# Performance work log

Measured on AMD Instinct MI355X. Metric: run time of the kernel, lower is better.

## Reference

```python
import jax, jax.numpy as jnp
import numpy as np

N_NODES = 50000

def cheb_conv(x, edge_index, W, b):
    # PyG ChebConv, K=2, normalization='sym', lambda_max=2.0 (default):
    # scaled Laplacian L_hat = (2/lambda_max)*L - I = -D^{-1/2} A D^{-1/2} (zero diag).
    # Tx_0 = x, Tx_1 = L_hat @ x ; out = Tx_0 @ W[0] + Tx_1 @ W[1] + b
    src, dst = edge_index[0], edge_index[1]
    ones = jnp.ones(src.shape[0], x.dtype)
    deg = jax.ops.segment_sum(ones, src, num_segments=N_NODES)
    dinv = jnp.where(deg > 0, 1.0 / jnp.sqrt(deg), 0.0)
    norm = -dinv[src] * dinv[dst]                                   # [E]
    tx1 = jax.ops.segment_sum(x[src] * norm[:, None], dst, num_segments=N_NODES)
    return x @ W[0] + tx1 @ W[1] + b

def setup_inputs() -> dict:
    key = jax.random.key(0)
    ks = jax.random.split(key, 12)
    IN, OUT, E, P = 128, 2, 800000, 400000
    return {
        "x": jax.random.normal(ks[0], (N_NODES, IN), jnp.float32),
        "edge_index": jax.random.randint(ks[1], (2, E), 0, N_NODES),
        "E_pos": jax.random.randint(ks[2], (2, P), 0, N_NODES),
        "neg_edge_index": jax.random.randint(ks[3], (2, P), 0, N_NODES),
        "W1": jax.random.normal(ks[4], (2, IN, 300), jnp.float32) * 0.05,
        "b1": jnp.zeros((300,), jnp.float32),
        "W2": jax.random.normal(ks[5], (2, 300, 100), jnp.float32) * 0.05,
        "b2": jnp.zeros((100,), jnp.float32),
        "W3": jax.random.normal(ks[6], (2, 100, OUT), jnp.float32) * 0.05,
        "b3": jnp.zeros((OUT,), jnp.float32),
        "lin1_W": jax.random.normal(ks[7], (100, IN), jnp.float32) * 0.05,
        "lin1_b": jnp.zeros((100,), jnp.float32),
        "lin2_W": jax.random.normal(ks[8], (100, IN), jnp.float32) * 0.05,
        "lin2_b": jnp.zeros((100,), jnp.float32),
        "c1": jnp.full((1,), 0.5, jnp.float32),
        "c2": jnp.full((1,), 0.5, jnp.float32),
    }

def reference(x, edge_index, E_pos, neg_edge_index, W1, b1, W2, b2, W3, b3,
              lin1_W, lin1_b, lin2_W, lin2_b, c1, c2):
    # eval mode: F.dropout and dropout_edge are identity
    x0 = x
    h = jax.nn.relu(cheb_conv(x0, edge_index, W1, b1))
    x1 = jax.nn.relu(cheb_conv(h, edge_index, W2, b2))
    x2 = x1 + jax.nn.relu(x0 @ lin1_W.T + lin1_b)
    z = x1 + jax.nn.relu(x0 @ lin2_W.T + lin2_b)
    pos_score = jnp.sum(z[E_pos[0]] * z[E_pos[1]], axis=1)              # [P]
    pos_loss = -jnp.mean(jnp.log(jax.nn.sigmoid(pos_score) + 1e-15))
    neg_score = jnp.sum(z[neg_edge_index[0]] * z[neg_edge_index[1]], axis=1)
    neg_loss = -jnp.mean(jnp.log(1.0 - jax.nn.sigmoid(neg_score) + 1e-15))
    r_loss = pos_loss + neg_loss
    out = cheb_conv(x2, edge_index, W3, b3)                             # [N, out_channels]
    return (out, r_loss, c1, c2)
```

## Files before the change

kernel.cpp:

```cpp
#include <hip/hip_runtime.h>
#include <math.h>


typedef unsigned short ushort_t;
typedef unsigned char u8;
typedef __attribute__((ext_vector_type(8))) __bf16 bf16x8;
typedef __attribute__((ext_vector_type(8))) short s16x8;
typedef __attribute__((ext_vector_type(4))) float f32x4;
typedef __attribute__((ext_vector_type(2))) float f32x2;

#define NB_H 64
#define HW 12500
#define PW 25000
#define LOSS_NB 1792

__device__ __forceinline__ f32x4 mfma16x16x32(s16x8 a, s16x8 b, f32x4 c) {
  return __builtin_amdgcn_mfma_f32_16x16x32_bf16(
      __builtin_bit_cast(bf16x8, a), __builtin_bit_cast(bf16x8, b), c, 0, 0, 0);
}
__device__ __forceinline__ ushort_t f2bf(float f) {
  union { float f; unsigned u; } c; c.f = f;
  unsigned r = (c.u + 0x7FFFu + ((c.u >> 16) & 1u)) >> 16;
  return (ushort_t)r;
}
__device__ __forceinline__ f32x2 cvt2lo(unsigned u) {
  return __builtin_amdgcn_cvt_pk_f32_fp8((int)u, false);
}
__device__ __forceinline__ f32x2 cvt2hi(unsigned u) {
  return __builtin_amdgcn_cvt_pk_f32_fp8((int)u, true);
}
__device__ __forceinline__ u8 f2fp8(float f) {
  return (u8)(__builtin_amdgcn_cvt_pk_fp8_f32(f, 0.f, 0, false) & 0xff);
}

template<int VAR, int NT, int KTOT>
__global__ __launch_bounds__(256) void gemm_mfma(
    const ushort_t* __restrict__ A0, const ushort_t* __restrict__ A1,
    const ushort_t* __restrict__ Wt,
    const float* __restrict__ bias0, const float* __restrict__ bias1,
    const float* __restrict__ x1,
    const float* __restrict__ W3c, const float* __restrict__ b3c,
    void* __restrict__ out0, void* __restrict__ out1,
    float* __restrict__ t0g, float* __restrict__ t1g, int M)
{
  constexpr int NF = NT / 32;
  __shared__ __align__(16) ushort_t As[64 * 40];
  __shared__ __align__(16) ushort_t Bs[NT * 40];
  __shared__ float w3s[400];
  const int tid  = threadIdx.x;
  const int lane = tid & 63, w = tid >> 6;
  const int m0 = blockIdx.x * 64;
  const int wm = (w & 1) * 32, wn = (w >> 1) * (NT / 2);
  if (VAR == 2) { for (int i = tid; i < 400; i += 256) w3s[i] = W3c[i]; }
  f32x4 acc[2][NF];
#pragma unroll
  for (int i = 0; i < 2; ++i)
#pragma unroll
    for (int j = 0; j < NF; ++j) acc[i][j] = (f32x4){0.f, 0.f, 0.f, 0.f};

  for (int k0 = 0; k0 < KTOT; k0 += 32) {
    {
      const int r = tid >> 2, c8 = (tid & 3) * 8;
      const int gm = m0 + r;
      uint4 v = {0u, 0u, 0u, 0u};
      if (gm < M) {
        if (VAR == 1) {
          const u8* s8 = (const u8*)A0 + (size_t)gm * 320 + k0 + c8;
          const uint2 r8 = *(const uint2*)s8;
          const f32x2 f0 = cvt2lo(r8.x), f1 = cvt2hi(r8.x);
          const f32x2 f2 = cvt2lo(r8.y), f3 = cvt2hi(r8.y);
          v.x = (unsigned)f2bf(f0.x) | ((unsigned)f2bf(f0.y) << 16);
          v.y = (unsigned)f2bf(f1.x) | ((unsigned)f2bf(f1.y) << 16);
          v.z = (unsigned)f2bf(f2.x) | ((unsigned)f2bf(f2.y) << 16);
          v.w = (unsigned)f2bf(f3.x) | ((unsigned)f2bf(f3.y) << 16);
        } else {
          const ushort_t* srcp;
          if (VAR == 0) srcp = (k0 < 128) ? A0 + (size_t)gm * 128 + k0 + c8
                                          : A1 + (size_t)gm * 128 + (k0 - 128) + c8;
          else srcp = A0 + (size_t)gm * 128 + k0 + c8;
          v = *(const uint4*)srcp;
        }
      }
      *(uint4*)&As[r * 40 + c8] = v;
    }
    {
      const int c8 = (tid & 3) * 8;
#pragma unroll
      for (int i = 0; i < (NT * 4 + 255) / 256; ++i) {
        const int r = (tid >> 2) + i * 64;
        if (r < NT)
          *(uint4*)&Bs[r * 40 + c8] = *(const uint4*)(Wt + (size_t)r * KTOT + k0 + c8);
      }
    }
    __syncthreads();
    s16x8 af[2], bfr[NF];
#pragma unroll
    for (int mi = 0; mi < 2; ++mi)
      af[mi] = *(const s16x8*)&As[(wm + mi * 16 + (lane & 15)) * 40 + (lane >> 4) * 8];
#pragma unroll
    for (int ni = 0; ni < NF; ++ni)
      bfr[ni] = *(const s16x8*)&Bs[(wn + ni * 16 + (lane & 15)) * 40 + (lane >> 4) * 8];
#pragma unroll
    for (int mi = 0; mi < 2; ++mi)
#pragma unroll
      for (int ni = 0; ni < NF; ++ni)
        acc[mi][ni] = mfma16x16x32(af[mi], bfr[ni], acc[mi][ni]);
    __syncthreads();
  }

  if (VAR == 2) {
#pragma unroll
    for (int mi = 0; mi < 2; ++mi)
#pragma unroll
      for (int r = 0; r < 4; ++r) {
        const int gRow = m0 + wm + mi * 16 + ((lane >> 4) << 2) + r;
        float p0 = 0.f, p1 = 0.f, p2 = 0.f, p3 = 0.f;
#pragma unroll
        for (int ni = 0; ni < NF; ++ni) {
          const int col = wn + ni * 16 + (lane & 15);
          const float v = acc[mi][ni][r];
          if (gRow < M) {
            if (col < 100) {
              const float x2v = x1[(size_t)gRow * 128 + col] + fmaxf(v + bias0[col], 0.f);
              p0 = fmaf(x2v, w3s[col * 2 + 0], p0);
              p1 = fmaf(x2v, w3s[col * 2 + 1], p1);
              p2 = fmaf(x2v, w3s[200 + col * 2 + 0], p2);
              p3 = fmaf(x2v, w3s[200 + col * 2 + 1], p3);
            } else if (col < 200) {
              const int c = col - 100;
              ((u8*)out1)[(size_t)gRow * 128 + c] =
                  f2fp8(x1[(size_t)gRow * 128 + c] + fmaxf(v + bias1[c], 0.f));
            }
          }
        }
        if (wn == 0) {
#pragma unroll
          for (int off = 8; off; off >>= 1) {
            p0 += __shfl_down(p0, off, 16);
            p1 += __shfl_down(p1, off, 16);
            p2 += __shfl_down(p2, off, 16);
            p3 += __shfl_down(p3, off, 16);
          }
          if ((lane & 15) == 0 && gRow < M) {
            t0g[(size_t)gRow * 2 + 0] = p0 + b3c[0];
            t0g[(size_t)gRow * 2 + 1] = p1 + b3c[1];
            t1g[(size_t)gRow * 2 + 0] = p2;
            t1g[(size_t)gRow * 2 + 1] = p3;
          }
        }
      }
  } else {
#pragma unroll
    for (int mi = 0; mi < 2; ++mi)
#pragma unroll
      for (int ni = 0; ni < NF; ++ni)
#pragma unroll
        for (int r = 0; r < 4; ++r) {
          const int gRow = m0 + wm + mi * 16 + ((lane >> 4) << 2) + r;
          const int col  = wn + ni * 16 + (lane & 15);
          if (gRow >= M) continue;
          const float v = acc[mi][ni][r];
          if (VAR == 0) {
            ((u8*)out0)[(size_t)gRow * 320 + col] =
                (col < 300) ? f2fp8(fmaxf(v + bias0[col], 0.f)) : (u8)0;
          } else {
            if (col < 100) ((float*)out0)[(size_t)gRow * 128 + col] = v + bias0[col];
            else if (col < 200) ((u8*)out1)[(size_t)gRow * 128 + (col - 100)] = f2fp8(v);
          }
        }
  }
}

__global__ __launch_bounds__(256) void prep(
    const int* __restrict__ src, const int* __restrict__ dst, int E, int M,
    unsigned* __restrict__ partS, unsigned* __restrict__ partD,
    ushort_t* __restrict__ rank,
    const float* __restrict__ x, ushort_t* __restrict__ xb,
    u8* __restrict__ xf8, int n4,
    const float* __restrict__ W1, const float* __restrict__ W2,
    const float* __restrict__ l1W, const float* __restrict__ l2W,
    ushort_t* __restrict__ W1t, ushort_t* __restrict__ W2t,
    ushort_t* __restrict__ Wlt)
{
  __shared__ unsigned hist[HW];
  const int blk = blockIdx.x;
  if (blk < 2 * NB_H) {
    const int isD = (blk >= NB_H);
    const int b = isD ? blk - NB_H : blk;
    const int* keys = isD ? dst : src;
    unsigned* part = isD ? partD : partS;
    const int cs = (E + NB_H - 1) / NB_H;
    const int e0 = b * cs;
    const int e1 = (e0 + cs < E) ? e0 + cs : E;
    for (int r = 0; r < 2; ++r) {
      const int klo = r * 2 * HW;
      for (int i = threadIdx.x; i < HW; i += 256) hist[i] = 0;
      __syncthreads();
      for (int e = e0 + threadIdx.x; e < e1; e += 256) {
        const int k = keys[e] - klo;
        if ((unsigned)k < (unsigned)(2 * HW)) {
          const unsigned old = atomicAdd(&hist[k >> 1], (k & 1) ? 0x10000u : 1u);
          if (isD) rank[e] = (ushort_t)((old >> ((k & 1) * 16)) & 0xffffu);
        }
      }
      __syncthreads();
      for (int i = threadIdx.x; i < HW; i += 256)
        part[(size_t)b * PW + r * HW + i] = hist[i];
      __syncthreads();
    }
    return;
  }
  const int i = (blk - 2 * NB_H) * 256 + threadIdx.x;
  if (i < n4) {
    const float4 v = ((const float4*)x)[i];
    ushort4 o; o.x = f2bf(v.x); o.y = f2bf(v.y); o.z = f2bf(v.z); o.w = f2bf(v.w);
    ((ushort4*)xb)[i] = o;
    int p = 0;
    p = __builtin_amdgcn_cvt_pk_fp8_f32(v.x, v.y, p, false);
    p = __builtin_amdgcn_cvt_pk_fp8_f32(v.z, v.w, p, true);
    ((unsigned*)xf8)[i] = (unsigned)p;
    return;
  }
  const int j = i - n4;
  if (j < 81920) {
    const int n = j >> 8, k = j & 255;
    float v = 0.f;
    if (n < 300) v = (k < 128) ? W1[k * 300 + n] : W1[38400 + (k - 128) * 300 + n];
    W1t[j] = f2bf(v);
  } else if (j < 153600) {
    const int jj = j - 81920;
    const int n = jj / 320, k = jj - n * 320;
    float v = 0.f;
    if (n < 200 && k < 300) v = W2[(n < 100 ? 0 : 30000) + k * 100 + (n % 100)];
    W2t[jj] = f2bf(v);
  } else if (j < 182272) {
    const int jj = j - 153600;
    const int n = jj >> 7, k = jj & 127;
    float v = 0.f;
    if (n < 100) v = l1W[n * 128 + k];
    else if (n < 200) v = l2W[(n - 100) * 128 + k];
    Wlt[jj] = f2bf(v);
  }
}

__global__ void scan_local(const unsigned* __restrict__ partS,
                           unsigned* __restrict__ partD,
                           float* __restrict__ dinv,
                           int* __restrict__ ptr, int* __restrict__ bsum, int n)
{
  __shared__ int tmp[256];
  const int i = blockIdx.x * 256 + threadIdx.x;
  const int lane = threadIdx.x & 63;
  unsigned ssum = 0, dtot = 0;
  if (i < n && (i & 1) == 0) {
    const int c = i >> 1;
    for (int b = 0; b < NB_H; b += 8) {
      unsigned sv[8];
#pragma unroll
      for (int q = 0; q < 8; ++q) sv[q] = partS[(size_t)(b + q) * PW + c];
#pragma unroll
      for (int q = 0; q < 8; ++q) ssum += sv[q];
    }
    unsigned run = 0;
    for (int b = 0; b < NB_H; b += 8) {
      unsigned dv[8];
#pragma unroll
      for (int q = 0; q < 8; ++q) dv[q] = partD[(size_t)(b + q) * PW + c];
#pragma unroll
      for (int q = 0; q < 8; ++q) { const unsigned pre = run; run += dv[q]; dv[q] = pre; }
#pragma unroll
      for (int q = 0; q < 8; ++q) partD[(size_t)(b + q) * PW + c] = dv[q];
    }
    dtot = run;
  }
  const unsigned sAll = __shfl(ssum, lane & ~1, 64);
  const unsigned dAll = __shfl(dtot, lane & ~1, 64);
  int v = 0;
  if (i < n) {
    const int hs = (i & 1) * 16;
    const unsigned dg = (sAll >> hs) & 0xffffu;
    dinv[i] = dg ? 1.f / sqrtf((float)dg) : 0.f;
    v = (int)((dAll >> hs) & 0xffffu);
  }
  tmp[threadIdx.x] = v;
  __syncthreads();
  for (int off = 1; off < 256; off <<= 1) {
    const int t = (threadIdx.x >= off) ? tmp[threadIdx.x - off] : 0;
    __syncthreads();
    tmp[threadIdx.x] += t;
    __syncthreads();
  }
  if (i < n) ptr[i] = tmp[threadIdx.x] - v;
  if (threadIdx.x == 255) bsum[blockIdx.x] = tmp[255];
}

__global__ void scan_add2(int* __restrict__ ptr, const int* __restrict__ bsum,
                          int n, int E, int nb, float* __restrict__ accs)
{
  __shared__ int tmp[256];
  const int v = (threadIdx.x < nb) ? bsum[threadIdx.x] : 0;
  tmp[threadIdx.x] = v;
  __syncthreads();
  for (int off = 1; off < 256; off <<= 1) {
    const int t = (threadIdx.x >= off) ? tmp[threadIdx.x - off] : 0;
    __syncthreads();
    tmp[threadIdx.x] += t;
    __syncthreads();
  }
  __syncthreads();
  const int offset = (blockIdx.x > 0) ? tmp[blockIdx.x - 1] : 0;
  const int i = blockIdx.x * 256 + threadIdx.x;
  if (i < n) ptr[i] += offset;
  if (i == 0) { ptr[n] = E; accs[0] = 0.f; accs[1] = 0.f; }
}

__global__ void fill_csr2(const int* __restrict__ src, const int* __restrict__ dst,
                          const float* __restrict__ dinv, const int* __restrict__ ptr,
                          const unsigned* __restrict__ base32,
                          const ushort_t* __restrict__ rank,
                          int2* __restrict__ csr, int E)
{
  const int e = blockIdx.x * 256 + threadIdx.x;
  if (e >= E) return;
  const int cs = (E + NB_H - 1) / NB_H;
  const int b = e / cs;
  const int s = src[e], d = dst[e];
  const unsigned bv = base32[(size_t)b * PW + (d >> 1)];
  const int base = (int)((bv >> ((d & 1) * 16)) & 0xffffu);
  const int pos = ptr[d] + base + (int)rank[e];
  const float w = -dinv[s] * dinv[d];
  csr[pos] = make_int2(s, __float_as_int(w));
}

#define ACCV(u, ww) { f32x2 t; \
  t = cvt2lo(u.x); a[0]  = fmaf(ww, t.x, a[0]);  a[1]  = fmaf(ww, t.y, a[1]);  \
  t = cvt2hi(u.x); a[2]  = fmaf(ww, t.x, a[2]);  a[3]  = fmaf(ww, t.y, a[3]);  \
  t = cvt2lo(u.y); a[4]  = fmaf(ww, t.x, a[4]);  a[5]  = fmaf(ww, t.y, a[5]);  \
  t = cvt2hi(u.y); a[6]  = fmaf(ww, t.x, a[6]);  a[7]  = fmaf(ww, t.y, a[7]);  \
  t = cvt2lo(u.z); a[8]  = fmaf(ww, t.x, a[8]);  a[9]  = fmaf(ww, t.y, a[9]);  \
  t = cvt2hi(u.z); a[10] = fmaf(ww, t.x, a[10]); a[11] = fmaf(ww, t.y, a[11]); \
  t = cvt2lo(u.w); a[12] = fmaf(ww, t.x, a[12]); a[13] = fmaf(ww, t.y, a[13]); \
  t = cvt2hi(u.w); a[14] = fmaf(ww, t.x, a[14]); a[15] = fmaf(ww, t.y, a[15]); }

__global__ __launch_bounds__(256) void gather128e(
    const u8* __restrict__ xf8, ushort_t* __restrict__ txb,
    const int* __restrict__ ptr, const int2* __restrict__ csr, int M)
{
  const int node = (blockIdx.x * 256 + threadIdx.x) >> 3;
  const int sub  = threadIdx.x & 7;
  if (node >= M) return;
  const int beg = ptr[node], end = ptr[node + 1];
  float a[16] = {};
  int p = beg;
  for (; p + 8 <= end; p += 8) {
    int2 e[8];
#pragma unroll
    for (int q = 0; q < 8; ++q) e[q] = csr[p + q];
    uint4 v[8];
#pragma unroll
    for (int q = 0; q < 8; ++q)
      v[q] = *(const uint4*)(xf8 + (size_t)e[q].x * 128 + sub * 16);
#pragma unroll
    for (int q = 0; q < 8; ++q) { const float wq = __int_as_float(e[q].y); ACCV(v[q], wq) }
  }
  for (; p < end; ++p) {
    const int2 eq = csr[p]; const float wq = __int_as_float(eq.y);
    const uint4 v = *(const uint4*)(xf8 + (size_t)eq.x * 128 + sub * 16);
    ACCV(v, wq)
  }
  uint4 o1, o2;
  o1.x = (unsigned)f2bf(a[0])  | ((unsigned)f2bf(a[1])  << 16);
  o1.y = (unsigned)f2bf(a[2])  | ((unsigned)f2bf(a[3])  << 16);
  o1.z = (unsigned)f2bf(a[4])  | ((unsigned)f2bf(a[5])  << 16);
  o1.w = (unsigned)f2bf(a[6])  | ((unsigned)f2bf(a[7])  << 16);
  o2.x = (unsigned)f2bf(a[8])  | ((unsigned)f2bf(a[9])  << 16);
  o2.y = (unsigned)f2bf(a[10]) | ((unsigned)f2bf(a[11]) << 16);
  o2.z = (unsigned)f2bf(a[12]) | ((unsigned)f2bf(a[13]) << 16);
  o2.w = (unsigned)f2bf(a[14]) | ((unsigned)f2bf(a[15]) << 16);
  ushort_t* dstp = txb + (size_t)node * 128 + sub * 16;
  *(uint4*)dstp = o1;
  *(uint4*)(dstp + 8) = o2;
}

__global__ __launch_bounds__(256) void gather100e_x1(
    const u8* __restrict__ Brh, float* __restrict__ Ar,
    const int* __restrict__ ptr, const int2* __restrict__ csr, int M)
{
  const int node = (blockIdx.x * 256 + threadIdx.x) >> 3;
  const int sub  = threadIdx.x & 7;
  if (node >= M) return;
  const int beg = ptr[node], end = ptr[node + 1];
  float a[16] = {};
  int p = beg;
  for (; p + 8 <= end; p += 8) {
    int2 e[8];
#pragma unroll
    for (int q = 0; q < 8; ++q) e[q] = csr[p + q];
    uint4 v[8];
#pragma unroll
    for (int q = 0; q < 8; ++q)
      v[q] = *(const uint4*)(Brh + (size_t)e[q].x * 128 + sub * 16);
#pragma unroll
    for (int q = 0; q < 8; ++q) { const float wq = __int_as_float(e[q].y); ACCV(v[q], wq) }
  }
  for (; p < end; ++p) {
    const int2 eq = csr[p]; const float wq = __int_as_float(eq.y);
    const uint4 v = *(const uint4*)(Brh + (size_t)eq.x * 128 + sub * 16);
    ACCV(v, wq)
  }
  float* dstp = Ar + (size_t)node * 128 + sub * 16;
#pragma unroll
  for (int q = 0; q < 4; ++q) {
    float4 b = *(const float4*)(dstp + q * 4);
    b.x = fmaxf(b.x + a[q * 4 + 0], 0.f);
    b.y = fmaxf(b.y + a[q * 4 + 1], 0.f);
    b.z = fmaxf(b.z + a[q * 4 + 2], 0.f);
    b.w = fmaxf(b.w + a[q * 4 + 3], 0.f);
    *(float4*)(dstp + q * 4) = b;
  }
}
#undef ACCV

__device__ __forceinline__ void maskrow(uint4& r, int sub) {
  if (sub >= 6) { r.y = 0u; r.z = 0u; r.w = 0u; if (sub == 7) r.x = 0u; }
}
#define DOTV(uu, vv, s) { f32x2 p_, q_; \
  p_ = cvt2lo(uu.x); q_ = cvt2lo(vv.x); s = fmaf(p_.x, q_.x, s); s = fmaf(p_.y, q_.y, s); \
  p_ = cvt2hi(uu.x); q_ = cvt2hi(vv.x); s = fmaf(p_.x, q_.x, s); s = fmaf(p_.y, q_.y, s); \
  p_ = cvt2lo(uu.y); q_ = cvt2lo(vv.y); s = fmaf(p_.x, q_.x, s); s = fmaf(p_.y, q_.y, s); \
  p_ = cvt2hi(uu.y); q_ = cvt2hi(vv.y); s = fmaf(p_.x, q_.x, s); s = fmaf(p_.y, q_.y, s); \
  p_ = cvt2lo(uu.z); q_ = cvt2lo(vv.z); s = fmaf(p_.x, q_.x, s); s = fmaf(p_.y, q_.y, s); \
  p_ = cvt2hi(uu.z); q_ = cvt2hi(vv.z); s = fmaf(p_.x, q_.x, s); s = fmaf(p_.y, q_.y, s); \
  p_ = cvt2lo(uu.w); q_ = cvt2lo(vv.w); s = fmaf(p_.x, q_.x, s); s = fmaf(p_.y, q_.y, s); \
  p_ = cvt2hi(uu.w); q_ = cvt2hi(vv.w); s = fmaf(p_.x, q_.x, s); s = fmaf(p_.y, q_.y, s); }

__global__ __launch_bounds__(256) void loss_g2(
    const u8* __restrict__ zf8, const int* __restrict__ ep,
    const int* __restrict__ en, int P, float* __restrict__ acc,
    const float* __restrict__ t1, const float* __restrict__ t0,
    const int* __restrict__ ptr, const int2* __restrict__ csr,
    float* __restrict__ out, int M)
{
  const int tid = threadIdx.x;
  if (blockIdx.x >= LOSS_NB) {
    const int i = (blockIdx.x - LOSS_NB) * 256 + tid;
    if (i >= M) return;
    float a0 = 0.f, a1 = 0.f;
    const int beg = ptr[i], end = ptr[i + 1];
    int p = beg;
    for (; p + 4 <= end; p += 4) {
      const int2 e0 = csr[p], e1 = csr[p + 1], e2 = csr[p + 2], e3 = csr[p + 3];
      const float w0 = __int_as_float(e0.y), w1 = __int_as_float(e1.y);
      const float w2 = __int_as_float(e2.y), w3 = __int_as_float(e3.y);
      const float2 v0 = *(const float2*)(t1 + (size_t)e0.x * 2);
      const float2 v1 = *(const float2*)(t1 + (size_t)e1.x * 2);
      const float2 v2 = *(const float2*)(t1 + (size_t)e2.x * 2);
      const float2 v3 = *(const float2*)(t1 + (size_t)e3.x * 2);
      a0 = fmaf(w0, v0.x, a0); a1 = fmaf(w0, v0.y, a1);
      a0 = fmaf(w1, v1.x, a0); a1 = fmaf(w1, v1.y, a1);
      a0 = fmaf(w2, v2.x, a0); a1 = fmaf(w2, v2.y, a1);
      a0 = fmaf(w3, v3.x, a0); a1 = fmaf(w3, v3.y, a1);
    }
    for (; p < end; ++p) {
      const int2 eq = csr[p]; const float wq = __int_as_float(eq.y);
      const float2 v = *(const float2*)(t1 + (size_t)eq.x * 2);
      a0 = fmaf(wq, v.x, a0); a1 = fmaf(wq, v.y, a1);
    }
    const float2 base = *(const float2*)(t0 + (size_t)i * 2);
    *(float2*)(out + (size_t)i * 2) = make_float2(base.x + a0, base.y + a1);
    return;
  }
  __shared__ float red[8];
  const int lane = tid & 63, wib = tid >> 6;
  const int sub = tid & 7;
  const int slot0 = blockIdx.x * 32 + (tid >> 3);
  const int step = LOSS_NB * 32;
  float tp = 0.f, tn = 0.f;
  int g = slot0;
  for (; g + 3 * step < 2 * P; g += 4 * step) {
    int neg[4], na[4], nb[4];
#pragma unroll
    for (int q = 0; q < 4; ++q) {
      const int gq = g + q * step;
      neg[q] = (gq >= P);
      const int p = neg[q] ? gq - P : gq;
      const int* ia = neg[q] ? en : ep;
      na[q] = ia[p]; nb[q] = ia[P + p];
    }
    uint4 ra[4], rb[4];
#pragma unroll
    for (int q = 0; q < 4; ++q) {
      ra[q] = make_uint4(0u, 0u, 0u, 0u);
      rb[q] = make_uint4(0u, 0u, 0u, 0u);
      if (sub < 7) {
        ra[q] = *(const uint4*)(zf8 + (size_t)na[q] * 128 + sub * 16);
        rb[q] = *(const uint4*)(zf8 + (size_t)nb[q] * 128 + sub * 16);
      }
      maskrow(ra[q], sub); maskrow(rb[q], sub);
    }
    float s[4] = {0.f, 0.f, 0.f, 0.f};
#pragma unroll
    for (int q = 0; q < 4; ++q) DOTV(ra[q], rb[q], s[q])
#pragma unroll
    for (int off = 4; off; off >>= 1) {
#pragma unroll
      for (int q = 0; q < 4; ++q) s[q] += __shfl_down(s[q], off, 8);
    }
    if (sub == 0) {
#pragma unroll
      for (int q = 0; q < 4; ++q) {
        const float sig = 1.f / (1.f + __expf(-s[q]));
        if (neg[q]) tn += __logf(1.f - sig + 1e-15f); else tp += __logf(sig + 1e-15f);
      }
    }
  }
  for (; g < 2 * P; g += step) {
    const int neg = (g >= P);
    const int p = neg ? g - P : g;
    const int* ia = neg ? en : ep;
    const int na = ia[p], nb = ia[P + p];
    uint4 ra = make_uint4(0u, 0u, 0u, 0u);
    uint4 rb = make_uint4(0u, 0u, 0u, 0u);
    if (sub < 7) {
      ra = *(const uint4*)(zf8 + (size_t)na * 128 + sub * 16);
      rb = *(const uint4*)(zf8 + (size_t)nb * 128 + sub * 16);
    }
    maskrow(ra, sub); maskrow(rb, sub);
    float s = 0.f;
    DOTV(ra, rb, s)
#pragma unroll
    for (int off = 4; off; off >>= 1) s += __shfl_down(s, off, 8);
    if (sub == 0) {
      const float sig = 1.f / (1.f + __expf(-s));
      if (neg) tn += __logf(1.f - sig + 1e-15f); else tp += __logf(sig + 1e-15f);
    }
  }
  tp += __shfl_down(tp, 32, 64); tn += __shfl_down(tn, 32, 64);
  tp += __shfl_down(tp, 16, 64); tn += __shfl_down(tn, 16, 64);
  tp += __shfl_down(tp, 8, 64);  tn += __shfl_down(tn, 8, 64);
  if (lane == 0) { red[wib] = tp; red[4 + wib] = tn; }
  __syncthreads();
  if (tid == 0) {
    atomicAdd(acc + 0, red[0] + red[1] + red[2] + red[3]);
    atomicAdd(acc + 1, red[4] + red[5] + red[6] + red[7]);
  }
}
#undef DOTV

__global__ void final_scalars(const float* __restrict__ accs,
                              const float* __restrict__ c1, const float* __restrict__ c2,
                              float* __restrict__ out, int M, float invP)
{
  out[2 * M + 0] = -(accs[0] + accs[1]) * invP;
  out[2 * M + 1] = c1[0];
  out[2 * M + 2] = c2[0];
}

extern "C" void kernel_launch(void* const* d_in, const int* in_sizes, int n_in,
                              void* d_out, int out_size, void* d_ws, size_t ws_size,
                              hipStream_t stream)
{
  const float* x   = (const float*)d_in[0];
  const int*   ei  = (const int*)d_in[1];
  const int*   ep  = (const int*)d_in[2];
  const int*   en  = (const int*)d_in[3];
  const float* W1  = (const float*)d_in[4];
  const float* b1  = (const float*)d_in[5];
  const float* W2  = (const float*)d_in[6];
  const float* b2  = (const float*)d_in[7];
  const float* W3  = (const float*)d_in[8];
  const float* b3  = (const float*)d_in[9];
  const float* l1W = (const float*)d_in[10];
  const float* l1b = (const float*)d_in[11];
  const float* l2W = (const float*)d_in[12];
  const float* l2b = (const float*)d_in[13];
  const float* c1  = (const float*)d_in[14];
  const float* c2  = (const float*)d_in[15];
  float* out = (float*)d_out;

  const int M = in_sizes[0] / 128;
  const int E = in_sizes[1] / 2;
  const int P = in_sizes[2] / 2;
  const int* src = ei;
  const int* dst = ei + E;
  const int nb_scan = (M + 255) / 256;

  float* ws = (float*)d_ws;
  size_t o = 0;
  float*    dinv = ws + o;            o += 50176;
  int*      cnt  = (int*)(ws + o);    o += (size_t)M;
  int*      ptr  = (int*)(ws + o);    o += (size_t)M + 8;
  int*      bsum = (int*)(ws + o);    o += 256;
  int2*     csr  = (int2*)(ws + o);   o += (size_t)E * 2;
  ushort_t* rank = (ushort_t*)(ws + o); o += (size_t)E / 2;
  ushort_t* xb   = (ushort_t*)(ws + o); o += (size_t)M * 64;
  u8*       xf8  = (u8*)(ws + o);     o += (size_t)M * 32;
  ushort_t* tx0b = (ushort_t*)(ws + o); o += (size_t)M * 64;
  ushort_t* W1t  = (ushort_t*)(ws + o); o += 40960;
  ushort_t* W2t  = (ushort_t*)(ws + o); o += 35840;
  ushort_t* Wlt  = (ushort_t*)(ws + o); o += 14336;
  u8*       h8   = (u8*)(ws + o);     o += (size_t)M * 160;
  float*    Ar   = ws + o;            o += (size_t)M * 128;
  u8*       Brh  = (u8*)(ws + o);     o += (size_t)M * 32;
  u8*       zf8  = (u8*)(ws + o);     o += (size_t)M * 32;
  float*    t0   = ws + o;            o += (size_t)M * 2;
  float*    t1   = ws + o;            o += (size_t)M * 2;
  float*    accs = ws + o;            o += 8;
  unsigned* partS = (unsigned*)h8;
  unsigned* partD = (unsigned*)Ar;

  const int n4 = M * 32;
  const int packBlocks = (n4 + 182272 + 255) / 256;
  prep<<<2 * NB_H + packBlocks, 256, 0, stream>>>(
      src, dst, E, M, partS, partD, rank,
      x, xb, xf8, n4, W1, W2, l1W, l2W, W1t, W2t, Wlt);

  scan_local<<<nb_scan, 256, 0, stream>>>(partS, partD, dinv, ptr, bsum, M);
  scan_add2<<<nb_scan, 256, 0, stream>>>(ptr, bsum, M, E, nb_scan, accs);
  fill_csr2<<<(E + 255) / 256, 256, 0, stream>>>(src, dst, dinv, ptr, partD, rank, csr, E);

  const int gB = (M + 63) / 64;
  const int gE8 = (M * 8 + 255) / 256;

  gather128e<<<gE8, 256, 0, stream>>>(xf8, tx0b, ptr, csr, M);
  gemm_mfma<0, 320, 256><<<gB, 256, 0, stream>>>(
      xb, tx0b, W1t, b1, nullptr, nullptr, nullptr, nullptr, h8, nullptr, nullptr, nullptr, M);

  gemm_mfma<1, 224, 320><<<gB, 256, 0, stream>>>(
      (const ushort_t*)h8, nullptr, W2t, b2, nullptr, nullptr, nullptr, nullptr,
      Ar, Brh, nullptr, nullptr, M);
  gather100e_x1<<<gE8, 256, 0, stream>>>(Brh, Ar, ptr, csr, M);

  gemm_mfma<2, 224, 128><<<gB, 256, 0, stream>>>(
      xb, nullptr, Wlt, l1b, l2b, Ar , W3, b3, nullptr, zf8, t0, t1, M);

  loss_g2<<<LOSS_NB + nb_scan, 256, 0, stream>>>(
      zf8, ep, en, P, accs, t1, t0, ptr, csr, out, M);
  final_scalars<<<1, 1, 0, stream>>>(accs, c1, c2, out, M, 1.0f / (float)P);
}
```

Baseline: 453.2 us.

## Bucket loss edge pairs by first node so each row of z is loaded once

Builds a CSR-like grouping of positive and negative pairs keyed by their first node. It reuses the histogram, scan and fill passes that already build the graph CSR, and stores a sign bit to mark negative pairs. The loss kernel then assigns eight lanes per node, loads and converts that node's fp8 row once, and computes dot products only against the partner rows. This removes half of the random gathers in the loss. In exchange it adds histogram, scan and fill work on the 800K pair indices, and per-node load imbalance across lanes.

```diff
diff --git a/kernel.cpp b/kernel.cpp
--- a/kernel.cpp
+++ b/kernel.cpp
@@ -12,7 +12,6 @@
 #define NB_H 64
 #define HW 12500
 #define PW 25000
-#define LOSS_NB 1792
 
 __device__ __forceinline__ f32x4 mfma16x16x32(s16x8 a, s16x8 b, f32x4 c) {
   return __builtin_amdgcn_mfma_f32_16x16x32_bf16(
@@ -175,6 +174,8 @@
     const int* __restrict__ src, const int* __restrict__ dst, int E, int M,
     unsigned* __restrict__ partS, unsigned* __restrict__ partD,
     ushort_t* __restrict__ rank,
+    const int* __restrict__ ep, const int* __restrict__ en, int P,
+    unsigned* __restrict__ partP, ushort_t* __restrict__ prank,
     const float* __restrict__ x, ushort_t* __restrict__ xb,
     u8* __restrict__ xf8, int n4,
     const float* __restrict__ W1, const float* __restrict__ W2,
@@ -210,7 +211,34 @@
     }
     return;
   }
-  const int i = (blk - 2 * NB_H) * 256 + threadIdx.x;
+  if (blk < 3 * NB_H) {
+    const int b = blk - 2 * NB_H;
+    const int twoP = 2 * P;
+    const int cs2 = (twoP + NB_H - 1) / NB_H;
+    const int e0 = b * cs2;
+    const int e1 = (e0 + cs2 < twoP) ? e0 + cs2 : twoP;
+    for (int r = 0; r < 2; ++r) {
+      const int klo = r * 2 * HW;
+      for (int i = threadIdx.x; i < HW; i += 256) hist[i] = 0;
+      __syncthreads();
+      for (int i = e0 + threadIdx.x; i < e1; i += 256) {
+        const int neg = (i >= P);
+        const int p = neg ? i - P : i;
+        const int* ia = neg ? en : ep;
+        const int k = ia[p] - klo;
+        if ((unsigned)k < (unsigned)(2 * HW)) {
+          const unsigned old = atomicAdd(&hist[k >> 1], (k & 1) ? 0x10000u : 1u);
+          prank[i] = (ushort_t)((old >> ((k & 1) * 16)) & 0xffffu);
+        }
+      }
+      __syncthreads();
+      for (int i = threadIdx.x; i < HW; i += 256)
+        partP[(size_t)b * PW + r * HW + i] = hist[i];
+      __syncthreads();
+    }
+    return;
+  }
+  const int i = (blk - 3 * NB_H) * 256 + threadIdx.x;
   if (i < n4) {
     const float4 v = ((const float4*)x)[i];
     ushort4 o; o.x = f2bf(v.x); o.y = f2bf(v.y); o.z = f2bf(v.z); o.w = f2bf(v.w);
@@ -245,13 +273,15 @@
 
 __global__ void scan_local(const unsigned* __restrict__ partS,
                            unsigned* __restrict__ partD,
+                           unsigned* __restrict__ partP,
                            float* __restrict__ dinv,
-                           int* __restrict__ ptr, int* __restrict__ bsum, int n)
+                           int* __restrict__ ptr, int* __restrict__ pptr,
+                           int* __restrict__ bsumE, int* __restrict__ bsumP, int n)
 {
   __shared__ int tmp[256];
   const int i = blockIdx.x * 256 + threadIdx.x;
   const int lane = threadIdx.x & 63;
-  unsigned ssum = 0, dtot = 0;
+  unsigned ssum = 0, dtot = 0, ptot = 0;
   if (i < n && (i & 1) == 0) {
     const int c = i >> 1;
     for (int b = 0; b < NB_H; b += 8) {
@@ -272,15 +302,28 @@
       for (int q = 0; q < 8; ++q) partD[(size_t)(b + q) * PW + c] = dv[q];
     }
     dtot = run;
+    unsigned prun = 0;
+    for (int b = 0; b < NB_H; b += 8) {
+      unsigned pv[8];
+#pragma unroll
+      for (int q = 0; q < 8; ++q) pv[q] = partP[(size_t)(b + q) * PW + c];
+#pragma unroll
+      for (int q = 0; q < 8; ++q) { const unsigned pre = prun; prun += pv[q]; pv[q] = pre; }
+#pragma unroll
+      for (int q = 0; q < 8; ++q) partP[(size_t)(b + q) * PW + c] = pv[q];
+    }
+    ptot = prun;
   }
   const unsigned sAll = __shfl(ssum, lane & ~1, 64);
   const unsigned dAll = __shfl(dtot, lane & ~1, 64);
-  int v = 0;
+  const unsigned pAll = __shfl(ptot, lane & ~1, 64);
+  int v = 0, v2 = 0;
   if (i < n) {
     const int hs = (i & 1) * 16;
     const unsigned dg = (sAll >> hs) & 0xffffu;
     dinv[i] = dg ? 1.f / sqrtf((float)dg) : 0.f;
     v = (int)((dAll >> hs) & 0xffffu);
+    v2 = (int)((pAll >> hs) & 0xffffu);
   }
   tmp[threadIdx.x] = v;
   __syncthreads();
@@ -291,14 +334,26 @@
     __syncthreads();
   }
   if (i < n) ptr[i] = tmp[threadIdx.x] - v;
-  if (threadIdx.x == 255) bsum[blockIdx.x] = tmp[255];
-}
-
-__global__ void scan_add2(int* __restrict__ ptr, const int* __restrict__ bsum,
-                          int n, int E, int nb, float* __restrict__ accs)
+  if (threadIdx.x == 255) bsumE[blockIdx.x] = tmp[255];
+  __syncthreads();
+  tmp[threadIdx.x] = v2;
+  __syncthreads();
+  for (int off = 1; off < 256; off <<= 1) {
+    const int t = (threadIdx.x >= off) ? tmp[threadIdx.x - off] : 0;
+    __syncthreads();
+    tmp[threadIdx.x] += t;
+    __syncthreads();
+  }
+  if (i < n) pptr[i] = tmp[threadIdx.x] - v2;
+  if (threadIdx.x == 255) bsumP[blockIdx.x] = tmp[255];
+}
+
+__global__ void scan_add2(int* __restrict__ ptr, int* __restrict__ pptr,
+                          const int* __restrict__ bsumE, const int* __restrict__ bsumP,
+                          int n, int E, int twoP, int nb, float* __restrict__ accs)
 {
   __shared__ int tmp[256];
-  const int v = (threadIdx.x < nb) ? bsum[threadIdx.x] : 0;
+  const int v = (threadIdx.x < nb) ? bsumE[threadIdx.x] : 0;
   tmp[threadIdx.x] = v;
   __syncthreads();
   for (int off = 1; off < 256; off <<= 1) {
@@ -307,29 +362,59 @@
     tmp[threadIdx.x] += t;
     __syncthreads();
   }
+  const int offE = (blockIdx.x > 0) ? tmp[blockIdx.x - 1] : 0;
   __syncthreads();
-  const int offset = (blockIdx.x > 0) ? tmp[blockIdx.x - 1] : 0;
+  const int v2 = (threadIdx.x < nb) ? bsumP[threadIdx.x] : 0;
+  tmp[threadIdx.x] = v2;
+  __syncthreads();
+  for (int off = 1; off < 256; off <<= 1) {
+    const int t = (threadIdx.x >= off) ? tmp[threadIdx.x - off] : 0;
+    __syncthreads();
+    tmp[threadIdx.x] += t;
+    __syncthreads();
+  }
+  const int offP = (blockIdx.x > 0) ? tmp[blockIdx.x - 1] : 0;
   const int i = blockIdx.x * 256 + threadIdx.x;
-  if (i < n) ptr[i] += offset;
-  if (i == 0) { ptr[n] = E; accs[0] = 0.f; accs[1] = 0.f; }
-}
-
-__global__ void fill_csr2(const int* __restrict__ src, const int* __restrict__ dst,
-                          const float* __restrict__ dinv, const int* __restrict__ ptr,
-                          const unsigned* __restrict__ base32,
-                          const ushort_t* __restrict__ rank,
-                          int2* __restrict__ csr, int E)
-{
-  const int e = blockIdx.x * 256 + threadIdx.x;
-  if (e >= E) return;
-  const int cs = (E + NB_H - 1) / NB_H;
-  const int b = e / cs;
-  const int s = src[e], d = dst[e];
-  const unsigned bv = base32[(size_t)b * PW + (d >> 1)];
-  const int base = (int)((bv >> ((d & 1) * 16)) & 0xffffu);
-  const int pos = ptr[d] + base + (int)rank[e];
-  const float w = -dinv[s] * dinv[d];
-  csr[pos] = make_int2(s, __float_as_int(w));
+  if (i < n) { ptr[i] += offE; pptr[i] += offP; }
+  if (i == 0) { ptr[n] = E; pptr[n] = twoP; accs[0] = 0.f; accs[1] = 0.f; }
+}
+
+__global__ __launch_bounds__(256) void fill2(
+    const int* __restrict__ src, const int* __restrict__ dst,
+    const float* __restrict__ dinv, const int* __restrict__ ptr,
+    const unsigned* __restrict__ baseD, const ushort_t* __restrict__ rank,
+    int2* __restrict__ csr, int E, int fillE,
+    const int* __restrict__ ep, const int* __restrict__ en, int P,
+    const int* __restrict__ pptr, const unsigned* __restrict__ baseP,
+    const ushort_t* __restrict__ prank, int* __restrict__ pnb)
+{
+  const int blk = blockIdx.x;
+  if (blk < fillE) {
+    const int e = blk * 256 + threadIdx.x;
+    if (e >= E) return;
+    const int cs = (E + NB_H - 1) / NB_H;
+    const int b = e / cs;
+    const int s = src[e], d = dst[e];
+    const unsigned bv = baseD[(size_t)b * PW + (d >> 1)];
+    const int base = (int)((bv >> ((d & 1) * 16)) & 0xffffu);
+    const int pos = ptr[d] + base + (int)rank[e];
+    const float w = -dinv[s] * dinv[d];
+    csr[pos] = make_int2(s, __float_as_int(w));
+    return;
+  }
+  const int i = (blk - fillE) * 256 + threadIdx.x;
+  const int twoP = 2 * P;
+  if (i >= twoP) return;
+  const int neg = (i >= P);
+  const int p = neg ? i - P : i;
+  const int* ia = neg ? en : ep;
+  const int na = ia[p], nbv = ia[P + p];
+  const int cs2 = (twoP + NB_H - 1) / NB_H;
+  const int b = i / cs2;
+  const unsigned bv = baseP[(size_t)b * PW + (na >> 1)];
+  const int base = (int)((bv >> ((na & 1) * 16)) & 0xffffu);
+  const int pos = pptr[na] + base + (int)prank[i];
+  pnb[pos] = nbv | (neg ? (int)0x80000000 : 0);
 }
 
 #define ACCV(u, ww) { f32x2 t; \
@@ -424,26 +509,26 @@
 __device__ __forceinline__ void maskrow(uint4& r, int sub) {
   if (sub >= 6) { r.y = 0u; r.z = 0u; r.w = 0u; if (sub == 7) r.x = 0u; }
 }
-#define DOTV(uu, vv, s) { f32x2 p_, q_; \
-  p_ = cvt2lo(uu.x); q_ = cvt2lo(vv.x); s = fmaf(p_.x, q_.x, s); s = fmaf(p_.y, q_.y, s); \
-  p_ = cvt2hi(uu.x); q_ = cvt2hi(vv.x); s = fmaf(p_.x, q_.x, s); s = fmaf(p_.y, q_.y, s); \
-  p_ = cvt2lo(uu.y); q_ = cvt2lo(vv.y); s = fmaf(p_.x, q_.x, s); s = fmaf(p_.y, q_.y, s); \
-  p_ = cvt2hi(uu.y); q_ = cvt2hi(vv.y); s = fmaf(p_.x, q_.x, s); s = fmaf(p_.y, q_.y, s); \
-  p_ = cvt2lo(uu.z); q_ = cvt2lo(vv.z); s = fmaf(p_.x, q_.x, s); s = fmaf(p_.y, q_.y, s); \
-  p_ = cvt2hi(uu.z); q_ = cvt2hi(vv.z); s = fmaf(p_.x, q_.x, s); s = fmaf(p_.y, q_.y, s); \
-  p_ = cvt2lo(uu.w); q_ = cvt2lo(vv.w); s = fmaf(p_.x, q_.x, s); s = fmaf(p_.y, q_.y, s); \
-  p_ = cvt2hi(uu.w); q_ = cvt2hi(vv.w); s = fmaf(p_.x, q_.x, s); s = fmaf(p_.y, q_.y, s); }
+#define DOTA(vv, s) { f32x2 q_; \
+  q_ = cvt2lo(vv.x); s = fmaf(af[0],  q_.x, s); s = fmaf(af[1],  q_.y, s); \
+  q_ = cvt2hi(vv.x); s = fmaf(af[2],  q_.x, s); s = fmaf(af[3],  q_.y, s); \
+  q_ = cvt2lo(vv.y); s = fmaf(af[4],  q_.x, s); s = fmaf(af[5],  q_.y, s); \
+  q_ = cvt2hi(vv.y); s = fmaf(af[6],  q_.x, s); s = fmaf(af[7],  q_.y, s); \
+  q_ = cvt2lo(vv.z); s = fmaf(af[8],  q_.x, s); s = fmaf(af[9],  q_.y, s); \
+  q_ = cvt2hi(vv.z); s = fmaf(af[10], q_.x, s); s = fmaf(af[11], q_.y, s); \
+  q_ = cvt2lo(vv.w); s = fmaf(af[12], q_.x, s); s = fmaf(af[13], q_.y, s); \
+  q_ = cvt2hi(vv.w); s = fmaf(af[14], q_.x, s); s = fmaf(af[15], q_.y, s); }
 
 __global__ __launch_bounds__(256) void loss_g2(
-    const u8* __restrict__ zf8, const int* __restrict__ ep,
-    const int* __restrict__ en, int P, float* __restrict__ acc,
+    const u8* __restrict__ zf8, const int* __restrict__ pptr,
+    const int* __restrict__ pnb, float* __restrict__ acc,
     const float* __restrict__ t1, const float* __restrict__ t0,
     const int* __restrict__ ptr, const int2* __restrict__ csr,
-    float* __restrict__ out, int M)
+    float* __restrict__ out, int M, int lossNB)
 {
   const int tid = threadIdx.x;
-  if (blockIdx.x >= LOSS_NB) {
-    const int i = (blockIdx.x - LOSS_NB) * 256 + tid;
+  if (blockIdx.x >= lossNB) {
+    const int i = (blockIdx.x - lossNB) * 256 + tid;
     if (i >= M) return;
     float a0 = 0.f, a1 = 0.f;
     const int beg = ptr[i], end = ptr[i + 1];
@@ -473,66 +558,68 @@
   __shared__ float red[8];
   const int lane = tid & 63, wib = tid >> 6;
   const int sub = tid & 7;
-  const int slot0 = blockIdx.x * 32 + (tid >> 3);
-  const int step = LOSS_NB * 32;
+  const int node = (blockIdx.x * 256 + tid) >> 3;
   float tp = 0.f, tn = 0.f;
-  int g = slot0;
-  for (; g + 3 * step < 2 * P; g += 4 * step) {
-    int neg[4], na[4], nb[4];
-#pragma unroll
-    for (int q = 0; q < 4; ++q) {
-      const int gq = g + q * step;
-      neg[q] = (gq >= P);
-      const int p = neg[q] ? gq - P : gq;
-      const int* ia = neg[q] ? en : ep;
-      na[q] = ia[p]; nb[q] = ia[P + p];
-    }
-    uint4 ra[4], rb[4];
-#pragma unroll
-    for (int q = 0; q < 4; ++q) {
-      ra[q] = make_uint4(0u, 0u, 0u, 0u);
-      rb[q] = make_uint4(0u, 0u, 0u, 0u);
-      if (sub < 7) {
-        ra[q] = *(const uint4*)(zf8 + (size_t)na[q] * 128 + sub * 16);
-        rb[q] = *(const uint4*)(zf8 + (size_t)nb[q] * 128 + sub * 16);
-      }
-      maskrow(ra[q], sub); maskrow(rb[q], sub);
-    }
-    float s[4] = {0.f, 0.f, 0.f, 0.f};
-#pragma unroll
-    for (int q = 0; q < 4; ++q) DOTV(ra[q], rb[q], s[q])
-#pragma unroll
-    for (int off = 4; off; off >>= 1) {
-#pragma unroll
-      for (int q = 0; q < 4; ++q) s[q] += __shfl_down(s[q], off, 8);
-    }
-    if (sub == 0) {
+  if (node < M) {
+    uint4 ra = make_uint4(0u, 0u, 0u, 0u);
+    if (sub < 7) ra = *(const uint4*)(zf8 + (size_t)node * 128 + sub * 16);
+    maskrow(ra, sub);
+    float af[16];
+    { f32x2 t;
+      t = cvt2lo(ra.x); af[0]  = t.x; af[1]  = t.y;
+      t = cvt2hi(ra.x); af[2]  = t.x; af[3]  = t.y;
+      t = cvt2lo(ra.y); af[4]  = t.x; af[5]  = t.y;
+      t = cvt2hi(ra.y); af[6]  = t.x; af[7]  = t.y;
+      t = cvt2lo(ra.z); af[8]  = t.x; af[9]  = t.y;
+      t = cvt2hi(ra.z); af[10] = t.x; af[11] = t.y;
+      t = cvt2lo(ra.w); af[12] = t.x; af[13] = t.y;
+      t = cvt2hi(ra.w); af[14] = t.x; af[15] = t.y; }
+    const int beg = pptr[node], end = pptr[node + 1];
+    int p = beg;
+    for (; p + 4 <= end; p += 4) {
+      int nb4[4];
+#pragma unroll
+      for (int q = 0; q < 4; ++q) nb4[q] = pnb[p + q];
+      uint4 rb[4];
 #pragma unroll
       for (int q = 0; q < 4; ++q) {
-        const float sig = 1.f / (1.f + __expf(-s[q]));
-        if (neg[q]) tn += __logf(1.f - sig + 1e-15f); else tp += __logf(sig + 1e-15f);
-      }
-    }
-  }
-  for (; g < 2 * P; g += step) {
-    const int neg = (g >= P);
-    const int p = neg ? g - P : g;
-    const int* ia = neg ? en : ep;
-    const int na = ia[p], nb = ia[P + p];
-    uint4 ra = make_uint4(0u, 0u, 0u, 0u);
-    uint4 rb = make_uint4(0u, 0u, 0u, 0u);
-    if (sub < 7) {
-      ra = *(const uint4*)(zf8 + (size_t)na * 128 + sub * 16);
-      rb = *(const uint4*)(zf8 + (size_t)nb * 128 + sub * 16);
-    }
-    maskrow(ra, sub); maskrow(rb, sub);
-    float s = 0.f;
-    DOTV(ra, rb, s)
-#pragma unroll
-    for (int off = 4; off; off >>= 1) s += __shfl_down(s, off, 8);
-    if (sub == 0) {
-      const float sig = 1.f / (1.f + __expf(-s));
-      if (neg) tn += __logf(1.f - sig + 1e-15f); else tp += __logf(sig + 1e-15f);
+        rb[q] = make_uint4(0u, 0u, 0u, 0u);
+        const int nv = nb4[q] & 0x7fffffff;
+        if (sub < 7) rb[q] = *(const uint4*)(zf8 + (size_t)nv * 128 + sub * 16);
+        maskrow(rb[q], sub);
+      }
+      float s[4] = {0.f, 0.f, 0.f, 0.f};
+#pragma unroll
+      for (int q = 0; q < 4; ++q) DOTA(rb[q], s[q])
+#pragma unroll
+      for (int off = 4; off; off >>= 1) {
+#pragma unroll
+        for (int q = 0; q < 4; ++q) s[q] += __shfl_down(s[q], off, 8);
+      }
+      if (sub == 0) {
+#pragma unroll
+        for (int q = 0; q < 4; ++q) {
+          const float sig = 1.f / (1.f + __expf(-s[q]));
+          if ((unsigned)nb4[q] >> 31) tn += __logf(1.f - sig + 1e-15f);
+          else tp += __logf(sig + 1e-15f);
+        }
+      }
+    }
+    for (; p < end; ++p) {
+      const int nbv = pnb[p];
+      const int nv = nbv & 0x7fffffff;
+      uint4 rb = make_uint4(0u, 0u, 0u, 0u);
+      if (sub < 7) rb = *(const uint4*)(zf8 + (size_t)nv * 128 + sub * 16);
+      maskrow(rb, sub);
+      float s = 0.f;
+      DOTA(rb, s)
+#pragma unroll
+      for (int off = 4; off; off >>= 1) s += __shfl_down(s, off, 8);
+      if (sub == 0) {
+        const float sig = 1.f / (1.f + __expf(-s));
+        if ((unsigned)nbv >> 31) tn += __logf(1.f - sig + 1e-15f);
+        else tp += __logf(sig + 1e-15f);
+      }
     }
   }
   tp += __shfl_down(tp, 32, 64); tn += __shfl_down(tn, 32, 64);
@@ -545,7 +632,7 @@
     atomicAdd(acc + 1, red[4] + red[5] + red[6] + red[7]);
   }
 }
-#undef DOTV
+#undef DOTA
 
 __global__ void final_scalars(const float* __restrict__ accs,
                               const float* __restrict__ c1, const float* __restrict__ c2,
@@ -584,15 +671,20 @@
   const int* src = ei;
   const int* dst = ei + E;
   const int nb_scan = (M + 255) / 256;
+  const int fillE = (E + 255) / 256;
+  const int fillP = (2 * P + 255) / 256;
+  const int lossNB = (M * 8 + 255) / 256;
 
   float* ws = (float*)d_ws;
   size_t o = 0;
   float*    dinv = ws + o;            o += 50176;
-  int*      cnt  = (int*)(ws + o);    o += (size_t)M;
   int*      ptr  = (int*)(ws + o);    o += (size_t)M + 8;
-  int*      bsum = (int*)(ws + o);    o += 256;
+  int*      pptr = (int*)(ws + o);    o += (size_t)M + 8;
+  int*      bsumE = (int*)(ws + o);   o += 256;
+  int*      bsumP = (int*)(ws + o);   o += 256;
   int2*     csr  = (int2*)(ws + o);   o += (size_t)E * 2;
   ushort_t* rank = (ushort_t*)(ws + o); o += (size_t)E / 2;
+  int*      pnb  = (int*)(ws + o);    o += (size_t)2 * P;
   ushort_t* xb   = (ushort_t*)(ws + o); o += (size_t)M * 64;
   u8*       xf8  = (u8*)(ws + o);     o += (size_t)M * 32;
   ushort_t* tx0b = (ushort_t*)(ws + o); o += (size_t)M * 64;
@@ -608,16 +700,23 @@
   float*    accs = ws + o;            o += 8;
   unsigned* partS = (unsigned*)h8;
   unsigned* partD = (unsigned*)Ar;
+  ushort_t* prank = tx0b;
+  unsigned* partP = (unsigned*)((char*)tx0b + (size_t)2 * P * 2);
 
   const int n4 = M * 32;
   const int packBlocks = (n4 + 182272 + 255) / 256;
-  prep<<<2 * NB_H + packBlocks, 256, 0, stream>>>(
+  prep<<<3 * NB_H + packBlocks, 256, 0, stream>>>(
       src, dst, E, M, partS, partD, rank,
+      ep, en, P, partP, prank,
       x, xb, xf8, n4, W1, W2, l1W, l2W, W1t, W2t, Wlt);
 
-  scan_local<<<nb_scan, 256, 0, stream>>>(partS, partD, dinv, ptr, bsum, M);
-  scan_add2<<<nb_scan, 256, 0, stream>>>(ptr, bsum, M, E, nb_scan, accs);
-  fill_csr2<<<(E + 255) / 256, 256, 0, stream>>>(src, dst, dinv, ptr, partD, rank, csr, E);
+  scan_local<<<nb_scan, 256, 0, stream>>>(partS, partD, partP, dinv, ptr, pptr,
+                                          bsumE, bsumP, M);
+  scan_add2<<<nb_scan, 256, 0, stream>>>(ptr, pptr, bsumE, bsumP, M, E, 2 * P,
+                                         nb_scan, accs);
+  fill2<<<fillE + fillP, 256, 0, stream>>>(
+      src, dst, dinv, ptr, partD, rank, csr, E, fillE,
+      ep, en, P, pptr, partP, prank, pnb);
 
   const int gB = (M + 63) / 64;
   const int gE8 = (M * 8 + 255) / 256;
@@ -634,7 +733,7 @@
   gemm_mfma<2, 224, 128><<<gB, 256, 0, stream>>>(
       xb, nullptr, Wlt, l1b, l2b, Ar , W3, b3, nullptr, zf8, t0, t1, M);
 
-  loss_g2<<<LOSS_NB + nb_scan, 256, 0, stream>>>(
-      zf8, ep, en, P, accs, t1, t0, ptr, csr, out, M);
+  loss_g2<<<lossNB + nb_scan, 256, 0, stream>>>(
+      zf8, pptr, pnb, accs, t1, t0, ptr, csr, out, M, lossNB);
   final_scalars<<<1, 1, 0, stream>>>(accs, c1, c2, out, M, 1.0f / (float)P);
 }
```

Measured after the change: 457.3 us. No clear change (+0.9%).
